# Performance work log

Measured on AMD Instinct MI355X. Metric: run time of the kernel, lower is better.

## Reference

```python
import jax, jax.numpy as jnp
import numpy as np

N = 100000   # source points
M = 100000   # query (also) points
E = 2000000  # radius-neighbor pairs (row: query idx, col: source idx)
FEAT = 64
OUT = 2


def _linear_params(key, fan_in, fan_out):
    kw, kb = jax.random.split(key)
    bound = 1.0 / np.sqrt(fan_in)
    w = jax.random.uniform(kw, (fan_in, fan_out), jnp.float32, -bound, bound)
    b = jax.random.uniform(kb, (fan_out,), jnp.float32, -bound, bound)
    return w, b


def setup_inputs() -> dict:
    key = jax.random.key(0)
    ks = jax.random.split(key, 10)
    pcd = jax.random.normal(ks[0], (N, 3), jnp.float32)
    feats = jax.random.normal(ks[1], (N, FEAT), jnp.float32)
    also_pts = jax.random.normal(ks[2], (M, 3), jnp.float32)
    also_labels = jax.random.randint(ks[3], (M,), 0, 2, jnp.int64)
    row = jax.random.randint(ks[4], (E,), 0, M, jnp.int64)
    col = jax.random.randint(ks[5], (E,), 0, N, jnp.int64)
    w_in, b_in = _linear_params(ks[6], FEAT + 3, FEAT)
    w1, b1 = _linear_params(ks[7], FEAT, FEAT)
    w2, b2 = _linear_params(ks[8], FEAT, FEAT)
    w_out, b_out = _linear_params(ks[9], FEAT, OUT)
    return {"pcd": pcd, "feats": feats, "also_pts": also_pts,
            "also_labels": also_labels, "row": row, "col": col,
            "w_in": w_in, "b_in": b_in, "w1": w1, "b1": b1,
            "w2": w2, "b2": b2, "w_out": w_out, "b_out": b_out}


def reference(pcd, feats, also_pts, also_labels, row, col,
              w_in, b_in, w1, b1, w2, b2, w_out, b_out):
    # gather: relative position of query vs neighbor, and neighbor latent
    pos_relative = also_pts[row] - pcd[col]          # (E, 3)
    latents_relative = feats[col]                    # (E, FEAT)
    x = jnp.concatenate([latents_relative, pos_relative], axis=1)  # (E, FEAT+3)
    x = x @ w_in + b_in                              # fc_in
    x = jax.nn.relu(x) @ w1 + b1                     # mlp layer 0 (act then linear)
    x = jax.nn.relu(x) @ w2 + b2                     # mlp layer 1
    x = x @ w_out + b_out                            # fc_out -> (E, 2)
    probs = jax.nn.softmax(x, axis=1)
    return probs, also_labels[row]
```

## Files before the change

### kernel.cpp

```cpp
#include <hip/hip_runtime.h>
#include <hip/hip_bf16.h>


typedef _Float16 half8 __attribute__((ext_vector_type(8)));
typedef _Float16 half2v __attribute__((ext_vector_type(2)));
typedef __fp16   fp16x2 __attribute__((ext_vector_type(2)));
typedef __attribute__((ext_vector_type(4))) float f32x4;

union U84h { uint4 u; half8 h; };
union UPH  { half2v h; fp16x2 f; int i; unsigned u; };

__device__ __forceinline__ half2v cvt2h(float a, float b) {
    UPH t;
    t.f = __builtin_amdgcn_cvt_pkrtz(a, b);
    return t.h;
}

__device__ __forceinline__ half8 relu8(half8 v) {
    half8 z;
#pragma unroll
    for (int i = 0; i < 8; ++i) z[i] = (_Float16)0.f;
    return __builtin_elementwise_max(v, z);
}

__global__ __launch_bounds__(256) void pack_fold(
    const float* __restrict__ w1, const float* __restrict__ w_in,
    const float* __restrict__ b1, const float* __restrict__ w2,
    const float* __restrict__ w_out, const float* __restrict__ b2,
    const float* __restrict__ b_out,
    _Float16* __restrict__ w1f, _Float16* __restrict__ wAf,
    _Float16* __restrict__ wpf, _Float16* __restrict__ w0h,
    _Float16* __restrict__ w1h, _Float16* __restrict__ b1h,
    float* __restrict__ bf) {
    int t = blockIdx.x * 256 + threadIdx.x;
    if (t < 4096) {
        int f = t >> 9, lane = (t >> 3) & 63, j = t & 7;
        int ntile = f >> 1, kstep = f & 1;
        int k = kstep * 32 + ((lane >> 4) << 3) + j;
        int n = ntile * 16 + (lane & 15);
        w1f[t] = (_Float16)w1[k * 64 + n];
    } else if (t < 10240) {
        int i = t - 4096;
        int f = i >> 9, lane = (i >> 3) & 63, j = i & 7;
        int ntile = f / 3, ks = f % 3;
        int n = ntile * 16 + (lane & 15);
        float v;
        if (ks < 2) {
            int k = ks * 32 + ((lane >> 4) << 3) + j;
            v = w_in[k * 64 + n];
        } else {
            v = ((lane >> 4) == 0 && j < 3) ? -w_in[(64 + j) * 64 + n] : 0.f;
        }
        wAf[i] = (_Float16)v;
    } else if (t < 13312) {
        int i = t - 10240;
        int d = i >> 10, ks = (i >> 9) & 1, lane = (i >> 3) & 63, j = i & 7;
        int k = ks * 32 + ((lane >> 4) << 3) + j;
        wpf[i] = (_Float16)w_in[(64 + d) * 64 + k];
    } else if (t < 13376) {
        int n = t - 13312;
        float s0 = 0.f, s1 = 0.f;
#pragma unroll
        for (int j = 0; j < 64; ++j) {
            s0 = fmaf(w2[n * 64 + j], w_out[j * 2 + 0], s0);
            s1 = fmaf(w2[n * 64 + j], w_out[j * 2 + 1], s1);
        }
        w0h[n] = (_Float16)s0;
        w1h[n] = (_Float16)s1;
    } else if (t < 13440) {
        int n = t - 13376;
        b1h[n] = (_Float16)b1[n];
    } else if (t == 13440) {
        float s0 = b_out[0], s1 = b_out[1];
#pragma unroll
        for (int j = 0; j < 64; ++j) {
            s0 = fmaf(b2[j], w_out[j * 2 + 0], s0);
            s1 = fmaf(b2[j], w_out[j * 2 + 1], s1);
        }
        bf[0] = s0; bf[1] = s1;
    }
}

__global__ __launch_bounds__(256) void precompute_S(
    const float* __restrict__ feats, const float* __restrict__ pcd,
    const float* __restrict__ b_in, const half8* __restrict__ wAf,
    _Float16* __restrict__ S, int N) {
    int lane = threadIdx.x & 63;
    int idx = lane & 15, g = lane >> 4;
    int base = (blockIdx.x * 4 + (threadIdx.x >> 6)) * 16;
    if (base >= N) return;

    half8 wa[12];
#pragma unroll
    for (int f = 0; f < 12; ++f) wa[f] = wAf[f * 64 + lane];

    int p = base + idx;
    int ps = p < N ? p : N - 1;
    const float4* fp = (const float4*)(feats + (size_t)ps * 64);
    float4 f0 = fp[2 * g], f1 = fp[2 * g + 1];
    float4 f2 = fp[8 + 2 * g], f3 = fp[8 + 2 * g + 1];
    half8 b0, b1v, b2v;
    b0[0]=(_Float16)f0.x; b0[1]=(_Float16)f0.y; b0[2]=(_Float16)f0.z; b0[3]=(_Float16)f0.w;
    b0[4]=(_Float16)f1.x; b0[5]=(_Float16)f1.y; b0[6]=(_Float16)f1.z; b0[7]=(_Float16)f1.w;
    b1v[0]=(_Float16)f2.x; b1v[1]=(_Float16)f2.y; b1v[2]=(_Float16)f2.z; b1v[3]=(_Float16)f2.w;
    b1v[4]=(_Float16)f3.x; b1v[5]=(_Float16)f3.y; b1v[6]=(_Float16)f3.z; b1v[7]=(_Float16)f3.w;
    float px = 0.f, py = 0.f, pz = 0.f;
    if (g == 0) {
        const float* pp = pcd + (size_t)ps * 3;
        px = pp[0]; py = pp[1]; pz = pp[2];
    }
#pragma unroll
    for (int i = 0; i < 8; ++i) b2v[i] = (_Float16)0.f;
    b2v[0] = (_Float16)px; b2v[1] = (_Float16)py; b2v[2] = (_Float16)pz;

#pragma unroll
    for (int tt = 0; tt < 4; ++tt) {
        f32x4 bi = *(const f32x4*)(b_in + tt * 16 + 4 * g);
        f32x4 acc;
        acc = __builtin_amdgcn_mfma_f32_16x16x32_f16(wa[tt * 3 + 0], b0, bi, 0, 0, 0);
        acc = __builtin_amdgcn_mfma_f32_16x16x32_f16(wa[tt * 3 + 1], b1v, acc, 0, 0, 0);
        acc = __builtin_amdgcn_mfma_f32_16x16x32_f16(wa[tt * 3 + 2], b2v, acc, 0, 0, 0);
        union { uint2 u; _Float16 h[4]; } o;
        o.h[0] = (_Float16)acc[0]; o.h[1] = (_Float16)acc[1];
        o.h[2] = (_Float16)acc[2]; o.h[3] = (_Float16)acc[3];
        if (p < N) *(uint2*)(S + (size_t)p * 64 + tt * 16 + 4 * g) = o.u;
    }
}

__global__ __launch_bounds__(256, 4) void edge_mfma(
    const _Float16* __restrict__ S, const float* __restrict__ also_pts,
    const int* __restrict__ row, const int* __restrict__ col,
    const int* __restrict__ labels,
    const half8* __restrict__ w1f, const half8* __restrict__ wpf,
    const unsigned* __restrict__ w0p, const unsigned* __restrict__ w1p,
    const unsigned* __restrict__ b1p, const float* __restrict__ bfold,
    float* __restrict__ out, int E, int ngroups) {
    __shared__ half8 wf_lds[8][64];
    {
        int t = threadIdx.x;
        wf_lds[t >> 6][t & 63] = w1f[t];
        wf_lds[(t + 256) >> 6][t & 63] = w1f[t + 256];
    }
    __syncthreads();

    int lane = threadIdx.x & 63;
    int idx  = lane & 15;
    int g    = lane >> 4;
    int gwave  = blockIdx.x * 4 + (threadIdx.x >> 6);
    int nwaves = gridDim.x * 4;
    if (gwave >= ngroups) return;

    half8 wpd[3][2];
#pragma unroll
    for (int d = 0; d < 3; ++d)
#pragma unroll
        for (int ks = 0; ks < 2; ++ks) wpd[d][ks] = wpf[(d * 2 + ks) * 64 + lane];
    UPH w0v[8], w1v[8], b1v[8];
#pragma unroll
    for (int tt = 0; tt < 4; ++tt)
#pragma unroll
        for (int h = 0; h < 2; ++h) {
            int i = tt * 8 + 2 * g + h;
            w0v[tt * 2 + h].u = w0p[i];
            w1v[tt * 2 + h].u = w1p[i];
            b1v[tt * 2 + h].u = b1p[i];
        }
    float bf0 = bfold[0], bf1 = bfold[1];
    half2v zero2 = {(_Float16)0.f, (_Float16)0.f};

    int grp = gwave, stride = nwaves;
    int es0 = (grp << 4) + idx; es0 = es0 < E ? es0 : E - 1;
    int r_c = row[es0], c_c = col[es0];
    const uint4* sp0 = (const uint4*)(S + (size_t)c_c * 64);
    uint4 s0_c = sp0[g], s1_c = sp0[4 + g];
    const float* ap0 = also_pts + (size_t)r_c * 3;
    float ax_c = ap0[0], ay_c = ap0[1], az_c = ap0[2];
    int lb_c = labels[r_c];

    int gn = grp + stride; gn = gn < ngroups ? gn : grp;
    int es1 = (gn << 4) + idx; es1 = es1 < E ? es1 : E - 1;
    int r_n = row[es1], c_n = col[es1];

    for (; grp < ngroups; grp += stride) {
        const uint4* spn = (const uint4*)(S + (size_t)c_n * 64);
        uint4 s0_n = spn[g], s1_n = spn[4 + g];
        const float* apn = also_pts + (size_t)r_n * 3;
        float ax_n = apn[0], ay_n = apn[1], az_n = apn[2];
        int lb_n = labels[r_n];
        int g2 = grp + 2 * stride; g2 = g2 < ngroups ? g2 : grp;
        int es2 = (g2 << 4) + idx; es2 = es2 < E ? es2 : E - 1;
        int r_2 = row[es2], c_2 = col[es2];

        int e = (grp << 4) + idx;
        bool eok = e < E;
        U84h s0u, s1u; s0u.u = s0_c; s1u.u = s1_c;
        _Float16 ah = (_Float16)ax_c, bh = (_Float16)ay_c, ch = (_Float16)az_c;
        half8 av = {ah, ah, ah, ah, ah, ah, ah, ah};
        half8 bv = {bh, bh, bh, bh, bh, bh, bh, bh};
        half8 cv = {ch, ch, ch, ch, ch, ch, ch, ch};
        half8 q0 = av * wpd[0][0] + bv * wpd[1][0] + cv * wpd[2][0];
        half8 q1 = av * wpd[0][1] + bv * wpd[1][1] + cv * wpd[2][1];
        half8 x0 = relu8(s0u.h + q0);
        half8 x1 = relu8(s1u.h + q1);

        f32x4 zero = {0.f, 0.f, 0.f, 0.f};
        f32x4 acc[4];
#pragma unroll
        for (int tt = 0; tt < 4; ++tt) {
            acc[tt] = __builtin_amdgcn_mfma_f32_16x16x32_f16(wf_lds[2 * tt][lane],     x0, zero, 0, 0, 0);
            acc[tt] = __builtin_amdgcn_mfma_f32_16x16x32_f16(wf_lds[2 * tt + 1][lane], x1, acc[tt], 0, 0, 0);
        }

        half2v p0 = zero2, p1 = zero2;
#pragma unroll
        for (int tt = 0; tt < 4; ++tt) {
            half2v h01 = cvt2h(acc[tt][0], acc[tt][1]);
            half2v h23 = cvt2h(acc[tt][2], acc[tt][3]);
            h01 = __builtin_elementwise_max(h01 + b1v[tt * 2 + 0].h, zero2);
            h23 = __builtin_elementwise_max(h23 + b1v[tt * 2 + 1].h, zero2);
            p0 += h01 * w0v[tt * 2 + 0].h + h23 * w0v[tt * 2 + 1].h;
            p1 += h01 * w1v[tt * 2 + 0].h + h23 * w1v[tt * 2 + 1].h;
        }
        UPH P0, P1, T;
        P0.h = p0; P1.h = p1;
        T.i = __shfl_xor(P0.i, 16); P0.h += T.h;
        T.i = __shfl_xor(P0.i, 32); P0.h += T.h;
        T.i = __shfl_xor(P1.i, 16); P1.h += T.h;
        T.i = __shfl_xor(P1.i, 32); P1.h += T.h;

        if (g == 0 && eok) {
            float l0 = (float)P0.h[0] + (float)P0.h[1] + bf0;
            float l1 = (float)P1.h[0] + (float)P1.h[1] + bf1;
            float mx = fmaxf(l0, l1);
            float e0 = __expf(l0 - mx);
            float e1 = __expf(l1 - mx);
            float inv = 1.f / (e0 + e1);
            *(float2*)(out + (size_t)e * 2) = make_float2(e0 * inv, e1 * inv);
            out[(size_t)2 * E + e] = (float)lb_c;
        }

        s0_c = s0_n; s1_c = s1_n;
        ax_c = ax_n; ay_c = ay_n; az_c = az_n;
        lb_c = lb_n;
        r_n = r_2; c_n = c_2;
    }
}

extern "C" void kernel_launch(void* const* d_in, const int* in_sizes, int n_in,
                              void* d_out, int out_size, void* d_ws, size_t ws_size,
                              hipStream_t stream) {
    const float* pcd      = (const float*)d_in[0];
    const float* feats    = (const float*)d_in[1];
    const float* also_pts = (const float*)d_in[2];
    const int*   labels   = (const int*)d_in[3];
    const int*   row      = (const int*)d_in[4];
    const int*   col      = (const int*)d_in[5];
    const float* w_in     = (const float*)d_in[6];
    const float* b_in     = (const float*)d_in[7];
    const float* w1       = (const float*)d_in[8];
    const float* b1       = (const float*)d_in[9];
    const float* w2       = (const float*)d_in[10];
    const float* b2       = (const float*)d_in[11];
    const float* w_out    = (const float*)d_in[12];
    const float* b_out    = (const float*)d_in[13];

    int N = in_sizes[0] / 3;
    int E = in_sizes[4];

    _Float16* Sb  = (_Float16*)d_ws;
    _Float16* w1f = Sb + (size_t)N * 64;
    _Float16* wAf = w1f + 4096;
    _Float16* wpf = wAf + 6144;
    _Float16* w0h = wpf + 3072;
    _Float16* w1h = w0h + 64;
    _Float16* b1h = w1h + 64;
    float*    bf  = (float*)(b1h + 64);

    pack_fold<<<53, 256, 0, stream>>>(w1, w_in, b1, w2, w_out, b2, b_out,
                                      w1f, wAf, wpf, w0h, w1h, b1h, bf);

    int ngroupsS = (N + 15) / 16;
    precompute_S<<<(ngroupsS + 3) / 4, 256, 0, stream>>>(
        feats, pcd, b_in, (const half8*)wAf, Sb, N);

    int ngroups = (E + 15) / 16;
    edge_mfma<<<2048, 256, 0, stream>>>(Sb, also_pts, row, col, labels,
                                        (const half8*)w1f, (const half8*)wpf,
                                        (const unsigned*)w0h, (const unsigned*)w1h,
                                        (const unsigned*)b1h, bf,
                                        (float*)d_out, E, ngroups);
}
```

Before: 81.83 us.

## Fold 2-class softmax into sigmoid, move weights to LDS, drop software prefetch

The two-logit softmax becomes a sigmoid of the logit difference, using a single folded weight vector and bias. That halves the final dot-product work and removes one shuffle reduction. Per-lane weights (wpd, w0/w1, b1) now live in shared memory, which frees registers, and launch_bounds rises to 6 waves per SIMD with a 1536-block grid. The manual two-stage prefetch of row/col/S is removed in favour of relying on higher occupancy to hide gather latency. The risk is more exposed memory latency plus extra LDS reads in the inner loop.

```diff
diff --git a/kernel.cpp b/kernel.cpp
--- a/kernel.cpp
+++ b/kernel.cpp
@@ -21,6 +21,10 @@
 #pragma unroll
     for (int i = 0; i < 8; ++i) z[i] = (_Float16)0.f;
     return __builtin_elementwise_max(v, z);
+}
+__device__ __forceinline__ half8 splat8h(_Float16 h) {
+    half8 r = {h, h, h, h, h, h, h, h};
+    return r;
 }
 
 __global__ __launch_bounds__(256) void pack_fold(
@@ -29,9 +33,8 @@
     const float* __restrict__ w_out, const float* __restrict__ b2,
     const float* __restrict__ b_out,
     _Float16* __restrict__ w1f, _Float16* __restrict__ wAf,
-    _Float16* __restrict__ wpf, _Float16* __restrict__ w0h,
-    _Float16* __restrict__ w1h, _Float16* __restrict__ b1h,
-    float* __restrict__ bf) {
+    _Float16* __restrict__ wpf, _Float16* __restrict__ wdh,
+    _Float16* __restrict__ b1h, float* __restrict__ bfd) {
     int t = blockIdx.x * 256 + threadIdx.x;
     if (t < 4096) {
         int f = t >> 9, lane = (t >> 3) & 63, j = t & 7;
@@ -59,25 +62,20 @@
         wpf[i] = (_Float16)w_in[(64 + d) * 64 + k];
     } else if (t < 13376) {
         int n = t - 13312;
-        float s0 = 0.f, s1 = 0.f;
-#pragma unroll
-        for (int j = 0; j < 64; ++j) {
-            s0 = fmaf(w2[n * 64 + j], w_out[j * 2 + 0], s0);
-            s1 = fmaf(w2[n * 64 + j], w_out[j * 2 + 1], s1);
-        }
-        w0h[n] = (_Float16)s0;
-        w1h[n] = (_Float16)s1;
+        float s = 0.f;
+#pragma unroll
+        for (int j = 0; j < 64; ++j)
+            s = fmaf(w2[n * 64 + j], w_out[j * 2 + 0] - w_out[j * 2 + 1], s);
+        wdh[n] = (_Float16)s;
     } else if (t < 13440) {
         int n = t - 13376;
         b1h[n] = (_Float16)b1[n];
     } else if (t == 13440) {
-        float s0 = b_out[0], s1 = b_out[1];
-#pragma unroll
-        for (int j = 0; j < 64; ++j) {
-            s0 = fmaf(b2[j], w_out[j * 2 + 0], s0);
-            s1 = fmaf(b2[j], w_out[j * 2 + 1], s1);
-        }
-        bf[0] = s0; bf[1] = s1;
+        float s = b_out[0] - b_out[1];
+#pragma unroll
+        for (int j = 0; j < 64; ++j)
+            s = fmaf(b2[j], w_out[j * 2 + 0] - w_out[j * 2 + 1], s);
+        bfd[0] = s;
     }
 }
 
@@ -127,79 +125,56 @@
     }
 }
 
-__global__ __launch_bounds__(256, 4) void edge_mfma(
+__global__ __launch_bounds__(256, 6) void edge_mfma(
     const _Float16* __restrict__ S, const float* __restrict__ also_pts,
     const int* __restrict__ row, const int* __restrict__ col,
     const int* __restrict__ labels,
     const half8* __restrict__ w1f, const half8* __restrict__ wpf,
-    const unsigned* __restrict__ w0p, const unsigned* __restrict__ w1p,
-    const unsigned* __restrict__ b1p, const float* __restrict__ bfold,
+    const unsigned* __restrict__ wdp, const unsigned* __restrict__ b1p,
+    const float* __restrict__ bfdp,
     float* __restrict__ out, int E, int ngroups) {
     __shared__ half8 wf_lds[8][64];
+    __shared__ half8 wpd_lds[6][64];
+    __shared__ unsigned wd_lds[32];
+    __shared__ unsigned b1_lds[32];
     {
         int t = threadIdx.x;
-        wf_lds[t >> 6][t & 63] = w1f[t];
-        wf_lds[(t + 256) >> 6][t & 63] = w1f[t + 256];
+        ((half8*)wf_lds)[t] = w1f[t];
+        ((half8*)wf_lds)[t + 256] = w1f[t + 256];
+        ((half8*)wpd_lds)[t] = wpf[t];
+        if (t < 128) ((half8*)wpd_lds)[t + 256] = wpf[t + 256];
+        if (t < 32) { wd_lds[t] = wdp[t]; b1_lds[t] = b1p[t]; }
     }
     __syncthreads();
 
     int lane = threadIdx.x & 63;
     int idx  = lane & 15;
     int g    = lane >> 4;
+    float bfd = bfdp[0];
+    half2v zero2 = {(_Float16)0.f, (_Float16)0.f};
+
     int gwave  = blockIdx.x * 4 + (threadIdx.x >> 6);
     int nwaves = gridDim.x * 4;
-    if (gwave >= ngroups) return;
-
-    half8 wpd[3][2];
-#pragma unroll
-    for (int d = 0; d < 3; ++d)
-#pragma unroll
-        for (int ks = 0; ks < 2; ++ks) wpd[d][ks] = wpf[(d * 2 + ks) * 64 + lane];
-    UPH w0v[8], w1v[8], b1v[8];
-#pragma unroll
-    for (int tt = 0; tt < 4; ++tt)
-#pragma unroll
-        for (int h = 0; h < 2; ++h) {
-            int i = tt * 8 + 2 * g + h;
-            w0v[tt * 2 + h].u = w0p[i];
-            w1v[tt * 2 + h].u = w1p[i];
-            b1v[tt * 2 + h].u = b1p[i];
-        }
-    float bf0 = bfold[0], bf1 = bfold[1];
-    half2v zero2 = {(_Float16)0.f, (_Float16)0.f};
-
-    int grp = gwave, stride = nwaves;
-    int es0 = (grp << 4) + idx; es0 = es0 < E ? es0 : E - 1;
-    int r_c = row[es0], c_c = col[es0];
-    const uint4* sp0 = (const uint4*)(S + (size_t)c_c * 64);
-    uint4 s0_c = sp0[g], s1_c = sp0[4 + g];
-    const float* ap0 = also_pts + (size_t)r_c * 3;
-    float ax_c = ap0[0], ay_c = ap0[1], az_c = ap0[2];
-    int lb_c = labels[r_c];
-
-    int gn = grp + stride; gn = gn < ngroups ? gn : grp;
-    int es1 = (gn << 4) + idx; es1 = es1 < E ? es1 : E - 1;
-    int r_n = row[es1], c_n = col[es1];
-
-    for (; grp < ngroups; grp += stride) {
-        const uint4* spn = (const uint4*)(S + (size_t)c_n * 64);
-        uint4 s0_n = spn[g], s1_n = spn[4 + g];
-        const float* apn = also_pts + (size_t)r_n * 3;
-        float ax_n = apn[0], ay_n = apn[1], az_n = apn[2];
-        int lb_n = labels[r_n];
-        int g2 = grp + 2 * stride; g2 = g2 < ngroups ? g2 : grp;
-        int es2 = (g2 << 4) + idx; es2 = es2 < E ? es2 : E - 1;
-        int r_2 = row[es2], c_2 = col[es2];
-
+
+    for (int grp = gwave; grp < ngroups; grp += nwaves) {
         int e = (grp << 4) + idx;
         bool eok = e < E;
-        U84h s0u, s1u; s0u.u = s0_c; s1u.u = s1_c;
-        _Float16 ah = (_Float16)ax_c, bh = (_Float16)ay_c, ch = (_Float16)az_c;
-        half8 av = {ah, ah, ah, ah, ah, ah, ah, ah};
-        half8 bv = {bh, bh, bh, bh, bh, bh, bh, bh};
-        half8 cv = {ch, ch, ch, ch, ch, ch, ch, ch};
-        half8 q0 = av * wpd[0][0] + bv * wpd[1][0] + cv * wpd[2][0];
-        half8 q1 = av * wpd[0][1] + bv * wpd[1][1] + cv * wpd[2][1];
+        int es = eok ? e : E - 1;
+        int r = row[es], c = col[es];
+
+        const uint4* sp = (const uint4*)(S + (size_t)c * 64);
+        U84h s0u, s1u;
+        s0u.u = sp[g];
+        s1u.u = sp[4 + g];
+        const float* ap = also_pts + (size_t)r * 3;
+        float ax = ap[0], ay = ap[1], az = ap[2];
+        int lb = labels[r];
+
+        half8 av = splat8h((_Float16)ax);
+        half8 bv = splat8h((_Float16)ay);
+        half8 cv = splat8h((_Float16)az);
+        half8 q0 = av * wpd_lds[0][lane] + bv * wpd_lds[2][lane] + cv * wpd_lds[4][lane];
+        half8 q1 = av * wpd_lds[1][lane] + bv * wpd_lds[3][lane] + cv * wpd_lds[5][lane];
         half8 x0 = relu8(s0u.h + q0);
         half8 x1 = relu8(s1u.h + q1);
 
@@ -211,38 +186,31 @@
             acc[tt] = __builtin_amdgcn_mfma_f32_16x16x32_f16(wf_lds[2 * tt + 1][lane], x1, acc[tt], 0, 0, 0);
         }
 
-        half2v p0 = zero2, p1 = zero2;
+        half2v pd = zero2;
 #pragma unroll
         for (int tt = 0; tt < 4; ++tt) {
+            UPH b0u, b1u, w0u, w1u;
+            int i0 = tt * 8 + 2 * g;
+            b0u.u = b1_lds[i0];     b1u.u = b1_lds[i0 + 1];
+            w0u.u = wd_lds[i0];     w1u.u = wd_lds[i0 + 1];
             half2v h01 = cvt2h(acc[tt][0], acc[tt][1]);
             half2v h23 = cvt2h(acc[tt][2], acc[tt][3]);
-            h01 = __builtin_elementwise_max(h01 + b1v[tt * 2 + 0].h, zero2);
-            h23 = __builtin_elementwise_max(h23 + b1v[tt * 2 + 1].h, zero2);
-            p0 += h01 * w0v[tt * 2 + 0].h + h23 * w0v[tt * 2 + 1].h;
-            p1 += h01 * w1v[tt * 2 + 0].h + h23 * w1v[tt * 2 + 1].h;
-        }
-        UPH P0, P1, T;
-        P0.h = p0; P1.h = p1;
-        T.i = __shfl_xor(P0.i, 16); P0.h += T.h;
-        T.i = __shfl_xor(P0.i, 32); P0.h += T.h;
-        T.i = __shfl_xor(P1.i, 16); P1.h += T.h;
-        T.i = __shfl_xor(P1.i, 32); P1.h += T.h;
+            h01 = __builtin_elementwise_max(h01 + b0u.h, zero2);
+            h23 = __builtin_elementwise_max(h23 + b1u.h, zero2);
+            pd += h01 * w0u.h + h23 * w1u.h;
+        }
+        UPH P, T;
+        P.h = pd;
+        T.i = __shfl_xor(P.i, 16); P.h += T.h;
+        T.i = __shfl_xor(P.i, 32); P.h += T.h;
 
         if (g == 0 && eok) {
-            float l0 = (float)P0.h[0] + (float)P0.h[1] + bf0;
-            float l1 = (float)P1.h[0] + (float)P1.h[1] + bf1;
-            float mx = fmaxf(l0, l1);
-            float e0 = __expf(l0 - mx);
-            float e1 = __expf(l1 - mx);
-            float inv = 1.f / (e0 + e1);
-            *(float2*)(out + (size_t)e * 2) = make_float2(e0 * inv, e1 * inv);
-            out[(size_t)2 * E + e] = (float)lb_c;
-        }
-
-        s0_c = s0_n; s1_c = s1_n;
-        ax_c = ax_n; ay_c = ay_n; az_c = az_n;
-        lb_c = lb_n;
-        r_n = r_2; c_n = c_2;
+            float l = (float)P.h[0] + (float)P.h[1];
+            float u = __expf(-(l + bfd));
+            float pa = 1.f / (1.f + u);
+            *(float2*)(out + (size_t)e * 2) = make_float2(pa, 1.f - pa);
+            out[(size_t)2 * E + e] = (float)lb;
+        }
     }
 }
 
@@ -271,22 +239,20 @@
     _Float16* w1f = Sb + (size_t)N * 64;
     _Float16* wAf = w1f + 4096;
     _Float16* wpf = wAf + 6144;
-    _Float16* w0h = wpf + 3072;
-    _Float16* w1h = w0h + 64;
-    _Float16* b1h = w1h + 64;
-    float*    bf  = (float*)(b1h + 64);
+    _Float16* wdh = wpf + 3072;
+    _Float16* b1h = wdh + 64;
+    float*    bfd = (float*)(b1h + 64);
 
     pack_fold<<<53, 256, 0, stream>>>(w1, w_in, b1, w2, w_out, b2, b_out,
-                                      w1f, wAf, wpf, w0h, w1h, b1h, bf);
+                                      w1f, wAf, wpf, wdh, b1h, bfd);
 
     int ngroupsS = (N + 15) / 16;
     precompute_S<<<(ngroupsS + 3) / 4, 256, 0, stream>>>(
         feats, pcd, b_in, (const half8*)wAf, Sb, N);
 
     int ngroups = (E + 15) / 16;
-    edge_mfma<<<2048, 256, 0, stream>>>(Sb, also_pts, row, col, labels,
+    edge_mfma<<<1536, 256, 0, stream>>>(Sb, also_pts, row, col, labels,
                                         (const half8*)w1f, (const half8*)wpf,
-                                        (const unsigned*)w0h, (const unsigned*)w1h,
-                                        (const unsigned*)b1h, bf,
-                                        (float*)d_out, E, ngroups);
-}
+                                        (const unsigned*)wdh, (const unsigned*)b1h,
+                                        bfd, (float*)d_out, E, ngroups);
+}
```

New measurement: 201.0 us. +145.6%, slower.
